# Kernel optimization log

Measured on AMD Instinct MI355X. Metric: run time of the kernel, lower is better.

## Reference

```python
import jax, jax.numpy as jnp
from jax import lax
import numpy as np

DIMNUMS = ('NCHW', 'OIHW', 'NCHW')
SCORE_THR = 0.6
IOU_THR = 0.5
STRIDE, CELL = 2.0, 12.0
IMG_OFFSET = 1.0e5  # > max coord, separates images for batched NMS


def _conv(x, w, b):
    y = lax.conv_general_dilated(x, w, (1, 1), 'VALID', dimension_numbers=DIMNUMS)
    return y + b[None, :, None, None]


def _prelu(x, a):
    return jnp.where(x >= 0, x, a[None, :, None, None] * x)


def _maxpool2_ceil(x):
    # MaxPool2d(2,2,ceil_mode=True): pad right/bottom so out = ceil(H/2)
    H, W = x.shape[2], x.shape[3]
    ph, pw = (-H) % 2, (-W) % 2
    return lax.reduce_window(x, -jnp.inf, lax.max, (1, 1, 2, 2), (1, 1, 2, 2),
                             [(0, 0), (0, 0), (0, ph), (0, pw)])


def _pnet(x, w1, b1, a1, w2, b2, a2, w3, b3, a3, w41, b41, w42, b42):
    h = _prelu(_conv(x, w1, b1), a1)
    h = _maxpool2_ceil(h)
    h = _prelu(_conv(h, w2, b2), a2)
    h = _prelu(_conv(h, w3, b3), a3)
    logits = _conv(h, w41, b41)            # [B,2,Hp,Wp]
    prob = jax.nn.softmax(logits, axis=1)[:, 1]  # [B,Hp,Wp]
    pred = _conv(h, w42, b42)              # [B,4,Hp,Wp]
    return pred, prob


def _greedy_nms(boxes, valid, thr):
    # boxes already sorted by descending score; valid marks admissible rows
    K = boxes.shape[0]
    x1, y1, x2, y2 = boxes[:, 0], boxes[:, 1], boxes[:, 2], boxes[:, 3]
    areas = (x2 - x1) * (y2 - y1)
    idxs = jnp.arange(K)

    def body(i, keep):
        bi = boxes[i]
        xx1 = jnp.maximum(bi[0], x1)
        yy1 = jnp.maximum(bi[1], y1)
        xx2 = jnp.minimum(bi[2], x2)
        yy2 = jnp.minimum(bi[3], y2)
        inter = jnp.maximum(xx2 - xx1, 0.0) * jnp.maximum(yy2 - yy1, 0.0)
        iou = inter / (areas[i] + areas - inter)
        sup = (iou > thr) & (idxs > i)
        return jnp.where(keep[i], keep & ~sup, keep)

    return lax.fori_loop(0, K, body, valid)


def _refine_bbox(boxes, pred):
    # plus_one=False variant (PNet stage)
    w = boxes[:, 2] - boxes[:, 0]
    h = boxes[:, 3] - boxes[:, 1]
    scale = jnp.stack([w, h, w, h], axis=1)
    return boxes + pred * scale


def _square_bbox(boxes):
    w = boxes[:, 2] - boxes[:, 0]
    h = boxes[:, 3] - boxes[:, 1]
    l = jnp.maximum(w, h)
    x1 = boxes[:, 0] + 0.5 * w - 0.5 * l
    y1 = boxes[:, 1] + 0.5 * h - 0.5 * l
    return jnp.stack([x1, y1, x1 + l, y1 + l], axis=1)


def setup_inputs() -> dict:
    key = jax.random.key(0)
    ks = jax.random.split(key, 16)
    B, H, W = 4, 1080, 1920
    f32 = jnp.float32
    d = {
        'x': jax.random.normal(ks[0], (B, 3, H, W), dtype=f32),
        'w1': jax.random.normal(ks[1], (10, 3, 3, 3), dtype=f32) * 0.1,
        'b1': jax.random.normal(ks[2], (10,), dtype=f32) * 0.1,
        'a1': jnp.full((10,), 0.25, dtype=f32),
        'w2': jax.random.normal(ks[3], (16, 10, 3, 3), dtype=f32) * 0.1,
        'b2': jax.random.normal(ks[4], (16,), dtype=f32) * 0.1,
        'a2': jnp.full((16,), 0.25, dtype=f32),
        'w3': jax.random.normal(ks[5], (32, 16, 3, 3), dtype=f32) * 0.1,
        'b3': jax.random.normal(ks[6], (32,), dtype=f32) * 0.1,
        'a3': jnp.full((32,), 0.25, dtype=f32),
        'w41': jax.random.normal(ks[7], (2, 32, 1, 1), dtype=f32) * 0.1,
        'b41': jax.random.normal(ks[8], (2,), dtype=f32) * 0.1,
        'w42': jax.random.normal(ks[9], (4, 32, 1, 1), dtype=f32) * 0.1,
        'b42': jax.random.normal(ks[10], (4,), dtype=f32) * 0.1,
        'k': 1024,
    }
    return d


def reference(x, w1, b1, a1, w2, b2, a2, w3, b3, a3, w41, b41, w42, b42, k):
    B = x.shape[0]
    pred, prob = _pnet(x, w1, b1, a1, w2, b2, a2, w3, b3, a3, w41, b41, w42, b42)
    Hp, Wp = prob.shape[1], prob.shape[2]

    # decode grid boxes: bb = (x=j, y=i); q1 = floor((2*bb+1)/scale), scale=1
    ys, xs = jnp.meshgrid(jnp.arange(Hp, dtype=jnp.float32),
                          jnp.arange(Wp, dtype=jnp.float32), indexing='ij')
    x1 = jnp.floor(STRIDE * xs + 1.0)
    y1 = jnp.floor(STRIDE * ys + 1.0)
    x2 = jnp.floor(STRIDE * xs + CELL)
    y2 = jnp.floor(STRIDE * ys + CELL)
    grid_boxes = jnp.stack([x1, y1, x2, y2], axis=-1).reshape(-1, 4)  # [Hp*Wp,4]

    N = Hp * Wp
    scores = prob.reshape(B * N)
    preds = pred.transpose(0, 2, 3, 1).reshape(B * N, 4)
    boxes = jnp.broadcast_to(grid_boxes[None], (B, N, 4)).reshape(B * N, 4)
    imgidx = jnp.repeat(jnp.arange(B), N)

    valid = scores >= SCORE_THR
    masked = jnp.where(valid, scores, -jnp.inf)
    vals, idx = lax.top_k(masked, k)

    tb = boxes[idx]
    tp = preds[idx]
    timg = imgidx[idx]
    tvalid = valid[idx]

    # batched NMS via per-image coordinate offset
    off = timg.astype(jnp.float32)[:, None] * IMG_OFFSET
    keep = _greedy_nms(tb + off, tvalid, IOU_THR)

    refined = _square_bbox(_refine_bbox(tb, tp))
    out = jnp.concatenate([refined, vals[:, None]], axis=1)  # [K,5]
    return jnp.where(keep[:, None], out, 0.0)
```

## Files before the change

### kernel.cpp

```cpp
#include <hip/hip_runtime.h>
#include <stdint.h>

using u32 = unsigned int;
using u64 = unsigned long long;

constexpr int BATCH = 4;
constexpr int H0 = 1080, W0 = 1920;
constexpr int HP = 539,  WP = 959;
constexpr int H2 = 537,  W2 = 957;
constexpr int H3 = 535,  W3 = 955;
constexpr int N3 = H3 * W3;
constexpr int TOT3 = BATCH * N3;
constexpr int KSEL = 1024;
constexpr int SORTCAP = 4096;
constexpr float SCORE_THR_C = 0.6f;
constexpr float IOU_THR_C = 0.5f;
constexpr float IMG_OFF = 100000.0f;

constexpr int T1RY = 34, T1CX = 30;
constexpr int C2TY = 34, C2TX = 30;
constexpr int C3TY = 34, C3TX = 30;

constexpr size_t align256(size_t x) { return (x + 255) & ~(size_t)255; }
constexpr size_t oP1   = 0;
constexpr size_t sP1   = (size_t)BATCH * 10 * HP * WP * 4;
constexpr size_t oC2   = align256(oP1 + sP1);
constexpr size_t sC2   = (size_t)BATCH * 16 * H2 * W2 * 4;
constexpr size_t oCand = align256(oC2 + sC2);
constexpr size_t sCand = (size_t)TOT3 * 8;
constexpr size_t oSort = align256(oCand + sCand);
constexpr size_t oSel  = align256(oSort + (size_t)SORTCAP * 8);
constexpr size_t oBox  = align256(oSel + (size_t)KSEL * 8);
constexpr size_t oSup  = align256(oBox + (size_t)KSEL * 16);
constexpr size_t oKeep = align256(oSup + (size_t)KSEL * 16 * 8);
constexpr size_t oMisc = align256(oKeep + 16 * 8);
constexpr int    MISC_WORDS = 16 + 2048;
constexpr size_t WS_NEEDED = oMisc + (size_t)MISC_WORDS * 4;

__device__ __forceinline__ int keybin(u64 key) {
  u32 khi = (u32)(key >> 32);
  int d = (int)(khi - 0xC0800000u);
  if (d < 0) d = 0;
  int bin = d >> 12;
  return bin > 2047 ? 2047 : bin;
}

__global__ __launch_bounds__(256) void k_conv1(
    const float* __restrict__ x, const float* __restrict__ w1,
    const float* __restrict__ b1, const float* __restrict__ a1,
    float* __restrict__ P1, u32* __restrict__ misc) {
  __shared__ float sm[6834];
  int tid = threadIdx.x;
  int blk = blockIdx.x;
  if (blk == 0) {
    for (int i = tid; i < MISC_WORDS; i += 256) misc[i] = 0;
  }
  int btx = blk % T1CX; int r1 = blk / T1CX; int bty = r1 % T1RY; int b = r1 / T1RY;
  int r0 = 16 * bty; if (r0 > 523) r0 = 523;
  int c0 = 32 * btx; if (c0 > 927) c0 = 927;

  const float* xb = x + (size_t)b * 3 * H0 * W0;
  for (int i = tid; i < 6732; i += 256) {
    int ci = i / 2244; int rem = i - ci * 2244; int row = rem / 66; int col = rem - row * 66;
    sm[ci * 2278 + row * 67 + col] =
        xb[(size_t)ci * H0 * W0 + (size_t)(2 * r0 + row) * W0 + (2 * c0 + col)];
  }
  __syncthreads();

  int pr = tid >> 4, pc = tid & 15;
  float acc[10][8];
  #pragma unroll
  for (int c = 0; c < 10; ++c) {
    float bb = b1[c];
    #pragma unroll
    for (int o = 0; o < 8; ++o) acc[c][o] = bb;
  }
  #pragma unroll 1
  for (int ci = 0; ci < 3; ++ci) {
    const float* sp = sm + ci * 2278 + (2 * pr) * 67 + 4 * pc;
    float in[4][6];
    #pragma unroll
    for (int iy = 0; iy < 4; ++iy)
      #pragma unroll
      for (int ix = 0; ix < 6; ++ix)
        in[iy][ix] = sp[iy * 67 + ix];
    #pragma unroll
    for (int c = 0; c < 10; ++c) {
      const float* wc = w1 + (c * 3 + ci) * 9;
      float w0v = wc[0], w1v = wc[1], w2v = wc[2], w3v = wc[3], w4v = wc[4],
            w5v = wc[5], w6v = wc[6], w7v = wc[7], w8v = wc[8];
      #pragma unroll
      for (int sr = 0; sr < 2; ++sr)
        #pragma unroll
        for (int sc = 0; sc < 4; ++sc) {
          float a = acc[c][sr * 4 + sc];
          a = fmaf(in[sr][sc],     w0v, a); a = fmaf(in[sr][sc+1],   w1v, a); a = fmaf(in[sr][sc+2],   w2v, a);
          a = fmaf(in[sr+1][sc],   w3v, a); a = fmaf(in[sr+1][sc+1], w4v, a); a = fmaf(in[sr+1][sc+2], w5v, a);
          a = fmaf(in[sr+2][sc],   w6v, a); a = fmaf(in[sr+2][sc+1], w7v, a); a = fmaf(in[sr+2][sc+2], w8v, a);
          acc[c][sr * 4 + sc] = a;
        }
    }
  }
  int gy = r0 + pr, gx = c0 + 2 * pc;
  size_t base = ((size_t)(b * 10) * HP + gy) * WP + gx;
  #pragma unroll
  for (int c = 0; c < 10; ++c) {
    float al = a1[c];
    float v[8];
    #pragma unroll
    for (int o = 0; o < 8; ++o) { float u = acc[c][o]; v[o] = u >= 0.0f ? u : al * u; }
    float m0 = fmaxf(fmaxf(v[0], v[1]), fmaxf(v[4], v[5]));
    float m1 = fmaxf(fmaxf(v[2], v[3]), fmaxf(v[6], v[7]));
    P1[base + (size_t)c * HP * WP]     = m0;
    P1[base + (size_t)c * HP * WP + 1] = m1;
  }
}

__global__ __launch_bounds__(256) void k_conv2(
    const float* __restrict__ P1, const float* __restrict__ w2,
    const float* __restrict__ b2, const float* __restrict__ a2,
    float* __restrict__ C2) {
  __shared__ float sm[6300];
  int tid = threadIdx.x;
  int blk = blockIdx.x;
  int tx = blk % C2TX; int r1 = blk / C2TX; int ty = r1 % C2TY; int b = r1 / C2TY;
  int r0 = 16 * ty; if (r0 > 521) r0 = 521;
  int c0 = 32 * tx; if (c0 > 925) c0 = 925;

  const float* Pb = P1 + (size_t)b * 10 * HP * WP;
  for (int i = tid; i < 6120; i += 256) {
    int ci = i / 612; int rem = i - ci * 612; int row = rem / 34; int col = rem - row * 34;
    sm[ci * 630 + row * 35 + col] =
        Pb[(size_t)ci * HP * WP + (size_t)(r0 + row) * WP + (c0 + col)];
  }
  __syncthreads();

  int lane = tid & 63;
  int wv = __builtin_amdgcn_readfirstlane(tid >> 6);
  int c_lo = wv * 4;
  int rr = lane >> 3;
  int gg = lane & 7;

  float acc[4][8];
  #pragma unroll
  for (int c = 0; c < 4; ++c) {
    float bb = b2[c_lo + c];
    #pragma unroll
    for (int o = 0; o < 8; ++o) acc[c][o] = bb;
  }
  #pragma unroll 1
  for (int ci = 0; ci < 10; ++ci) {
    const float* sp = sm + ci * 630 + (2 * rr) * 35 + 4 * gg;
    float in[4][6];
    #pragma unroll
    for (int dy = 0; dy < 4; ++dy)
      #pragma unroll
      for (int dx = 0; dx < 6; ++dx)
        in[dy][dx] = sp[dy * 35 + dx];
    #pragma unroll
    for (int c = 0; c < 4; ++c) {
      const float* wc = w2 + ((c_lo + c) * 10 + ci) * 9;
      float w0v = wc[0], w1v = wc[1], w2v = wc[2], w3v = wc[3], w4v = wc[4],
            w5v = wc[5], w6v = wc[6], w7v = wc[7], w8v = wc[8];
      #pragma unroll
      for (int d = 0; d < 2; ++d)
        #pragma unroll
        for (int k = 0; k < 4; ++k) {
          float a = acc[c][d * 4 + k];
          a = fmaf(in[d][k],   w0v, a); a = fmaf(in[d][k+1],   w1v, a); a = fmaf(in[d][k+2],   w2v, a);
          a = fmaf(in[d+1][k], w3v, a); a = fmaf(in[d+1][k+1], w4v, a); a = fmaf(in[d+1][k+2], w5v, a);
          a = fmaf(in[d+2][k], w6v, a); a = fmaf(in[d+2][k+1], w7v, a); a = fmaf(in[d+2][k+2], w8v, a);
          acc[c][d * 4 + k] = a;
        }
    }
  }
  #pragma unroll
  for (int c = 0; c < 4; ++c) {
    float al = a2[c_lo + c];
    #pragma unroll
    for (int d = 0; d < 2; ++d) {
      int gy = r0 + 2 * rr + d;
      size_t base = ((size_t)(b * 16 + c_lo + c) * H2 + gy) * W2 + (c0 + 4 * gg);
      #pragma unroll
      for (int k = 0; k < 4; ++k) {
        float v = acc[c][d * 4 + k];
        C2[base + k] = v >= 0.0f ? v : al * v;
      }
    }
  }
}

__device__ __forceinline__ void conv3_h(
    const float* __restrict__ C2, const float* __restrict__ w3,
    const float* __restrict__ b3, const float* __restrict__ a3,
    int b, int y, int x, float* h) {
  #pragma unroll
  for (int c = 0; c < 32; ++c) h[c] = b3[c];
  #pragma unroll 1
  for (int ci = 0; ci < 16; ++ci) {
    const float* p = C2 + ((size_t)(b * 16 + ci) * H2 + y) * W2 + x;
    float i0 = p[0],      i1 = p[1],      i2 = p[2];
    float i3 = p[W2],     i4 = p[W2+1],   i5 = p[W2+2];
    float i6 = p[2*W2],   i7 = p[2*W2+1], i8 = p[2*W2+2];
    const float* wp = w3 + ci * 9;
    #pragma unroll
    for (int c = 0; c < 32; ++c) {
      const float* wc = wp + c * 144;
      h[c] = fmaf(i0, wc[0], h[c]); h[c] = fmaf(i1, wc[1], h[c]);
      h[c] = fmaf(i2, wc[2], h[c]); h[c] = fmaf(i3, wc[3], h[c]);
      h[c] = fmaf(i4, wc[4], h[c]); h[c] = fmaf(i5, wc[5], h[c]);
      h[c] = fmaf(i6, wc[6], h[c]); h[c] = fmaf(i7, wc[7], h[c]);
      h[c] = fmaf(i8, wc[8], h[c]);
    }
  }
  #pragma unroll
  for (int c = 0; c < 32; ++c) h[c] = h[c] >= 0.0f ? h[c] : a3[c] * h[c];
}

__global__ __launch_bounds__(256) void k_conv3(
    const float* __restrict__ C2, const float* __restrict__ w3,
    const float* __restrict__ b3, const float* __restrict__ a3,
    const float* __restrict__ w41, const float* __restrict__ b41,
    u64* __restrict__ cands, u32* __restrict__ misc) {
  __shared__ __align__(16) float sm[10080];
  int tid = threadIdx.x;
  int blk = blockIdx.x;
  int tx = blk % C3TX; int r1 = blk / C3TX; int ty = r1 % C3TY; int b = r1 / C3TY;
  int ymin = 16 * ty, xmin = 32 * tx;
  int r0 = ymin > 519 ? 519 : ymin;
  int c0 = xmin > 923 ? 923 : xmin;

  const float* Cb = C2 + (size_t)b * 16 * H2 * W2;
  for (int i = tid; i < 9792; i += 256) {
    int ci = i / 612; int rem = i - ci * 612; int row = rem / 34; int col = rem - row * 34;
    sm[ci * 630 + row * 35 + col] =
        Cb[(size_t)ci * H2 * W2 + (size_t)(r0 + row) * W2 + (c0 + col)];
  }
  __syncthreads();

  int lane = tid & 63;
  int wv = __builtin_amdgcn_readfirstlane(tid >> 6);
  int c_lo = wv * 8;
  int rr = lane >> 3;
  int gg = lane & 7;

  float acc[8][8];
  #pragma unroll
  for (int c = 0; c < 8; ++c) {
    float bb = b3[c_lo + c];
    #pragma unroll
    for (int o = 0; o < 8; ++o) acc[c][o] = bb;
  }
  #pragma unroll 1
  for (int ci = 0; ci < 16; ++ci) {
    const float* sp = sm + ci * 630 + (2 * rr) * 35 + 4 * gg;
    float in[4][6];
    #pragma unroll
    for (int dy = 0; dy < 4; ++dy)
      #pragma unroll
      for (int dx = 0; dx < 6; ++dx)
        in[dy][dx] = sp[dy * 35 + dx];
    #pragma unroll
    for (int c = 0; c < 8; ++c) {
      const float* wc = w3 + ((c_lo + c) * 16 + ci) * 9;
      float w0v = wc[0], w1v = wc[1], w2v = wc[2], w3v = wc[3], w4v = wc[4],
            w5v = wc[5], w6v = wc[6], w7v = wc[7], w8v = wc[8];
      #pragma unroll
      for (int d = 0; d < 2; ++d)
        #pragma unroll
        for (int k = 0; k < 4; ++k) {
          float a = acc[c][d * 4 + k];
          a = fmaf(in[d][k],   w0v, a); a = fmaf(in[d][k+1],   w1v, a); a = fmaf(in[d][k+2],   w2v, a);
          a = fmaf(in[d+1][k], w3v, a); a = fmaf(in[d+1][k+1], w4v, a); a = fmaf(in[d+1][k+2], w5v, a);
          a = fmaf(in[d+2][k], w6v, a); a = fmaf(in[d+2][k+1], w7v, a); a = fmaf(in[d+2][k+2], w8v, a);
          acc[c][d * 4 + k] = a;
        }
    }
  }
  #pragma unroll
  for (int c = 0; c < 8; ++c) {
    float al = a3[c_lo + c];
    #pragma unroll
    for (int o = 0; o < 8; ++o) {
      float v = acc[c][o];
      acc[c][o] = v >= 0.0f ? v : al * v;
    }
  }
  __syncthreads();

  #pragma unroll
  for (int halfp = 0; halfp < 2; ++halfp) {
    if ((rr >> 2) == halfp) {
      #pragma unroll
      for (int c = 0; c < 8; ++c)
        #pragma unroll
        for (int d = 0; d < 2; ++d) {
          int row = 2 * rr + d - 8 * halfp;
          int word = (c_lo + c) * 256 + row * 32 + 4 * gg;
          *(float4*)&sm[word] = make_float4(acc[c][d*4+0], acc[c][d*4+1], acc[c][d*4+2], acc[c][d*4+3]);
        }
    }
    __syncthreads();
    {
      int p = tid;
      float l0 = b41[0], l1 = b41[1];
      #pragma unroll
      for (int c = 0; c < 32; ++c) {
        float hv = sm[c * 256 + p];
        l0 = fmaf(hv, w41[c],      l0);
        l1 = fmaf(hv, w41[32 + c], l1);
      }
      float prob = 1.0f / (1.0f + expf(l0 - l1));
      int gy = r0 + 8 * halfp + (p >> 5);
      int gx = c0 + (p & 31);
      if (prob >= SCORE_THR_C && gy >= ymin && gx >= xmin) {
        u32 idx = (u32)(b * N3 + gy * W3 + gx);
        u64 key = ((u64)(~__float_as_uint(prob)) << 32) | idx;
        atomicAdd(&misc[16 + keybin(key)], 1u);
        u32 pos = atomicAdd(&misc[0], 1u);
        cands[pos] = key;
      }
    }
    __syncthreads();
  }
}

__global__ __launch_bounds__(256) void k_compact(const u64* __restrict__ cands,
                                                u32* __restrict__ misc,
                                                u64* __restrict__ sortbuf) {
  __shared__ u32 lh[2048];
  __shared__ u32 part[256];
  __shared__ u32 sb;
  int tid = threadIdx.x;
  const u32* hist = misc + 16;
  for (int t = tid; t < 2048; t += 256) lh[t] = hist[t];
  __syncthreads();
  u32 s = 0;
  #pragma unroll
  for (int k = 0; k < 8; ++k) s += lh[tid * 8 + k];
  part[tid] = s;
  __syncthreads();
  if (tid == 0) {
    u32 total = misc[0]; if (total > (u32)TOT3) total = TOT3;
    u32 keff = total < (u32)KSEL ? total : (u32)KSEL;
    u32 run = 0; int chunk = 255;
    for (int t = 0; t < 256; ++t) {
      if (run + part[t] >= keff) { chunk = t; break; }
      run += part[t];
    }
    int bstar = 2047;
    for (int b = chunk * 8; b < chunk * 8 + 8; ++b) {
      u32 hv = lh[b];
      if (run + hv >= keff) { bstar = b; break; }
      run += hv;
    }
    sb = (u32)bstar;
    if (blockIdx.x == 0) { misc[2] = (u32)bstar; misc[3] = keff; }
  }
  __syncthreads();
  int bstar = (int)sb;
  u32 n = misc[0]; if (n > (u32)TOT3) n = TOT3;
  u32 stride = gridDim.x * 256;
  for (u32 i = blockIdx.x * 256 + tid; i < n; i += stride) {
    u64 key = cands[i];
    if (keybin(key) <= bstar) {
      u32 pos = atomicAdd(&misc[1], 1u);
      if (pos < (u32)SORTCAP) sortbuf[pos] = key;
    }
  }
}

__global__ __launch_bounds__(1024) void k_sort(const u64* __restrict__ sortbuf,
                                               const u32* __restrict__ misc,
                                               u64* __restrict__ selected,
                                               float4* __restrict__ boxarr) {
  __shared__ u64 s[SORTCAP];
  int tid = threadIdx.x;
  u32 nsel = misc[1]; if (nsel > (u32)SORTCAP) nsel = SORTCAP;
  unsigned m = KSEL;
  while (m < nsel) m <<= 1;
  for (int t = tid; t < (int)m; t += 1024) s[t] = (t < (int)nsel) ? sortbuf[t] : ~0ULL;
  for (unsigned k = 2; k <= m; k <<= 1) {
    for (unsigned j = k >> 1; j > 0; j >>= 1) {
      __syncthreads();
      for (int t = tid; t < (int)m; t += 1024) {
        int ixj = t ^ (int)j;
        if (ixj > t) {
          u64 a = s[t], b = s[ixj];
          bool up = ((t & (int)k) == 0);
          if ((a > b) == up) { s[t] = b; s[ixj] = a; }
        }
      }
    }
  }
  __syncthreads();
  if (tid < KSEL) {
    u64 key = s[tid];
    selected[tid] = key;
    u32 idx = (u32)key;
    u32 b = idx / (u32)N3;
    u32 rem = idx - b * (u32)N3;
    u32 y = rem / (u32)W3;
    u32 x = rem - y * (u32)W3;
    float off = (float)b * IMG_OFF;
    float x1 = (float)(2 * (int)x + 1) + off;
    float y1 = (float)(2 * (int)y + 1) + off;
    boxarr[tid] = make_float4(x1, y1, x1 + 11.0f, y1 + 11.0f);
  }
}

__global__ __launch_bounds__(256) void k_sup(const float4* __restrict__ boxarr,
                                             u64* __restrict__ sup) {
  __shared__ float4 lbox[KSEL];
  int tid = threadIdx.x;
  for (int t = tid; t < KSEL; t += 256) lbox[t] = boxarr[t];
  __syncthreads();
  int i = blockIdx.x * 16 + (tid >> 4);
  int w = tid & 15;
  float4 bi = lbox[i];
  float ai = (bi.z - bi.x) * (bi.w - bi.y);
  u64 m = 0;
  #pragma unroll 4
  for (int jj = 0; jj < 64; ++jj) {
    int j = (w << 6) + jj;
    float4 bj = lbox[j];
    float xx1 = fmaxf(bi.x, bj.x), yy1 = fmaxf(bi.y, bj.y);
    float xx2 = fminf(bi.z, bj.z), yy2 = fminf(bi.w, bj.w);
    float inter = fmaxf(xx2 - xx1, 0.0f) * fmaxf(yy2 - yy1, 0.0f);
    float aj = (bj.z - bj.x) * (bj.w - bj.y);
    float iou = inter / (ai + aj - inter);
    if (iou > IOU_THR_C && j > i) m |= (1ULL << jj);
  }
  sup[(size_t)i * 16 + w] = m;
}

__global__ __launch_bounds__(256) void k_nms(const u64* __restrict__ sup,
                                             const u32* __restrict__ misc,
                                             u64* __restrict__ keep) {
  __shared__ u64 lsup[512 * 16];
  __shared__ u64 rem[16];
  __shared__ u64 keepres[16];
  int tid = threadIdx.x;
  int lane = tid & 63;
  int total = (int)misc[3];
  if (tid < 16) {
    rem[tid] = 0;
    int nb = total - tid * 64;
    keepres[tid] = nb >= 64 ? ~0ULL : (nb <= 0 ? 0ULL : ((1ULL << nb) - 1ULL));
  }
  for (int chunk = 0; chunk < 2; ++chunk) {
    for (int t = tid; t < 512 * 16; t += 256) lsup[t] = sup[(size_t)chunk * 512 * 16 + t];
    __syncthreads();
    for (int jb = 0; jb < 8; ++jb) {
      int j = chunk * 8 + jb;
      if (tid < 64) {
        u64 intra = lsup[(jb * 64 + lane) * 16 + j];
        u64 kw = keepres[j] & ~rem[j];
        #pragma unroll 8
        for (int bbit = 0; bbit < 64; ++bbit) {
          u64 row = __shfl(intra, bbit);
          if ((kw >> bbit) & 1ULL) kw &= ~row;
        }
        if (lane == 0) keepres[j] = kw;
      }
      __syncthreads();
      if (tid < 16) {
        u64 kw = keepres[j];
        u64 r = rem[tid];
        int base = jb * 64;
        while (kw) {
          int bbit = __ffsll(kw) - 1;
          kw &= kw - 1;
          r |= lsup[(base + bbit) * 16 + tid];
        }
        rem[tid] = r;
      }
      __syncthreads();
    }
  }
  if (tid < 16) keep[tid] = keepres[tid];
}

__global__ __launch_bounds__(256) void k_emit(
    const float* __restrict__ C2, const float* __restrict__ w3,
    const float* __restrict__ b3, const float* __restrict__ a3,
    const float* __restrict__ w42, const float* __restrict__ b42,
    const u64* __restrict__ selected, const u64* __restrict__ keep,
    float* __restrict__ out) {
  int r = blockIdx.x * 256 + threadIdx.x;
  if (r >= KSEL) return;
  bool kb = (keep[r >> 6] >> (r & 63)) & 1ULL;
  if (!kb) {
    out[r*5+0] = 0.0f; out[r*5+1] = 0.0f; out[r*5+2] = 0.0f;
    out[r*5+3] = 0.0f; out[r*5+4] = 0.0f;
    return;
  }
  u64 key = selected[r];
  float score = __uint_as_float(~(u32)(key >> 32));
  u32 idx = (u32)key;
  int b = (int)(idx / (u32)N3);
  int rem = (int)(idx - (u32)b * (u32)N3);
  int y = rem / W3;
  int x = rem - y * W3;
  float h[32];
  conv3_h(C2, w3, b3, a3, b, y, x, h);
  float p0 = b42[0], p1 = b42[1], p2 = b42[2], p3 = b42[3];
  #pragma unroll
  for (int c = 0; c < 32; ++c) {
    p0 = fmaf(h[c], w42[c],      p0);
    p1 = fmaf(h[c], w42[32 + c], p1);
    p2 = fmaf(h[c], w42[64 + c], p2);
    p3 = fmaf(h[c], w42[96 + c], p3);
  }
  float x1 = (float)(2 * x + 1), y1f = (float)(2 * y + 1);
  float x2 = (float)(2 * x + 12), y2f = (float)(2 * y + 12);
  float bw = x2 - x1, bh = y2f - y1f;
  float rx1 = fmaf(p0, bw, x1), ry1 = fmaf(p1, bh, y1f);
  float rx2 = fmaf(p2, bw, x2), ry2 = fmaf(p3, bh, y2f);
  float rw = rx2 - rx1, rh = ry2 - ry1;
  float l = fmaxf(rw, rh);
  float ox1 = rx1 + 0.5f * rw - 0.5f * l;
  float oy1 = ry1 + 0.5f * rh - 0.5f * l;
  out[r*5+0] = ox1; out[r*5+1] = oy1;
  out[r*5+2] = ox1 + l; out[r*5+3] = oy1 + l;
  out[r*5+4] = score;
}

extern "C" void kernel_launch(void* const* d_in, const int* in_sizes, int n_in,
                              void* d_out, int out_size, void* d_ws, size_t ws_size,
                              hipStream_t stream) {
  if (ws_size < WS_NEEDED) return;
  const float* x   = (const float*)d_in[0];
  const float* w1  = (const float*)d_in[1];
  const float* b1  = (const float*)d_in[2];
  const float* a1  = (const float*)d_in[3];
  const float* w2  = (const float*)d_in[4];
  const float* b2  = (const float*)d_in[5];
  const float* a2  = (const float*)d_in[6];
  const float* w3  = (const float*)d_in[7];
  const float* b3  = (const float*)d_in[8];
  const float* a3  = (const float*)d_in[9];
  const float* w41 = (const float*)d_in[10];
  const float* b41 = (const float*)d_in[11];
  const float* w42 = (const float*)d_in[12];
  const float* b42 = (const float*)d_in[13];

  char* ws = (char*)d_ws;
  float*  P1       = (float*)(ws + oP1);
  float*  C2       = (float*)(ws + oC2);
  u64*    cands    = (u64*)(ws + oCand);
  u64*    sortbuf  = (u64*)(ws + oSort);
  u64*    selected = (u64*)(ws + oSel);
  float4* boxarr   = (float4*)(ws + oBox);
  u64*    sup      = (u64*)(ws + oSup);
  u64*    keep     = (u64*)(ws + oKeep);
  u32*    misc     = (u32*)(ws + oMisc);
  float*  out      = (float*)d_out;

  k_conv1<<<T1RY * T1CX * BATCH, 256, 0, stream>>>(x, w1, b1, a1, P1, misc);
  k_conv2<<<C2TX * C2TY * BATCH, 256, 0, stream>>>(P1, w2, b2, a2, C2);
  k_conv3<<<C3TX * C3TY * BATCH, 256, 0, stream>>>(C2, w3, b3, a3, w41, b41, cands, misc);
  k_compact<<<512, 256, 0, stream>>>(cands, misc, sortbuf);
  k_sort<<<1, 1024, 0, stream>>>(sortbuf, misc, selected, boxarr);
  k_sup<<<64, 256, 0, stream>>>(boxarr, sup);
  k_nms<<<1, 256, 0, stream>>>(sup, misc, keep);
  k_emit<<<(KSEL + 255) / 256, 256, 0, stream>>>(C2, w3, b3, a3, w42, b42, selected, keep, out);
}
```

Before: 618.5 us.

## Fuse compact, sort, suppression-mask and NMS kernels into one single-block tail kernel

```diff
diff --git a/kernel.cpp b/kernel.cpp
--- a/kernel.cpp
+++ b/kernel.cpp
@@ -28,11 +28,8 @@
 constexpr size_t sC2   = (size_t)BATCH * 16 * H2 * W2 * 4;
 constexpr size_t oCand = align256(oC2 + sC2);
 constexpr size_t sCand = (size_t)TOT3 * 8;
-constexpr size_t oSort = align256(oCand + sCand);
-constexpr size_t oSel  = align256(oSort + (size_t)SORTCAP * 8);
-constexpr size_t oBox  = align256(oSel + (size_t)KSEL * 8);
-constexpr size_t oSup  = align256(oBox + (size_t)KSEL * 16);
-constexpr size_t oKeep = align256(oSup + (size_t)KSEL * 16 * 8);
+constexpr size_t oSel  = align256(oCand + sCand);
+constexpr size_t oKeep = align256(oSel + (size_t)KSEL * 8);
 constexpr size_t oMisc = align256(oKeep + 16 * 8);
 constexpr int    MISC_WORDS = 16 + 2048;
 constexpr size_t WS_NEEDED = oMisc + (size_t)MISC_WORDS * 4;
@@ -325,20 +322,29 @@
   }
 }
 
-__global__ __launch_bounds__(256) void k_compact(const u64* __restrict__ cands,
-                                                u32* __restrict__ misc,
-                                                u64* __restrict__ sortbuf) {
-  __shared__ u32 lh[2048];
-  __shared__ u32 part[256];
-  __shared__ u32 sb;
+__global__ __launch_bounds__(1024) void k_tail(
+    const u64* __restrict__ cands, u32* __restrict__ misc,
+    u64* __restrict__ selected, u64* __restrict__ keep) {
+  __shared__ __align__(16) char smraw[99328];
+  u64*    sbuf = (u64*)smraw;
+  u64*    lsup = (u64*)(smraw + 8192);
+  float4* lbox = (float4*)(smraw + 73728);
+  u32*    lh   = (u32*)(smraw + 90112);
+  u32*    part = (u32*)(smraw + 98304);
+  __shared__ u32 s_bstar, s_keff, s_cnt;
+  __shared__ u64 remw[16], keepres[16];
   int tid = threadIdx.x;
-  const u32* hist = misc + 16;
-  for (int t = tid; t < 2048; t += 256) lh[t] = hist[t];
-  __syncthreads();
-  u32 s = 0;
-  #pragma unroll
-  for (int k = 0; k < 8; ++k) s += lh[tid * 8 + k];
-  part[tid] = s;
+  int lane = tid & 63;
+
+  for (int t = tid; t < 2048; t += 1024) lh[t] = misc[16 + t];
+  if (tid == 0) s_cnt = 0;
+  __syncthreads();
+  if (tid < 256) {
+    u32 s = 0;
+    #pragma unroll
+    for (int k = 0; k < 8; ++k) s += lh[tid * 8 + k];
+    part[tid] = s;
+  }
   __syncthreads();
   if (tid == 0) {
     u32 total = misc[0]; if (total > (u32)TOT3) total = TOT3;
@@ -354,48 +360,45 @@
       if (run + hv >= keff) { bstar = b; break; }
       run += hv;
     }
-    sb = (u32)bstar;
-    if (blockIdx.x == 0) { misc[2] = (u32)bstar; misc[3] = keff; }
-  }
-  __syncthreads();
-  int bstar = (int)sb;
-  u32 n = misc[0]; if (n > (u32)TOT3) n = TOT3;
-  u32 stride = gridDim.x * 256;
-  for (u32 i = blockIdx.x * 256 + tid; i < n; i += stride) {
-    u64 key = cands[i];
-    if (keybin(key) <= bstar) {
-      u32 pos = atomicAdd(&misc[1], 1u);
-      if (pos < (u32)SORTCAP) sortbuf[pos] = key;
-    }
-  }
-}
-
-__global__ __launch_bounds__(1024) void k_sort(const u64* __restrict__ sortbuf,
-                                               const u32* __restrict__ misc,
-                                               u64* __restrict__ selected,
-                                               float4* __restrict__ boxarr) {
-  __shared__ u64 s[SORTCAP];
-  int tid = threadIdx.x;
-  u32 nsel = misc[1]; if (nsel > (u32)SORTCAP) nsel = SORTCAP;
+    s_bstar = (u32)bstar;
+    s_keff = keff;
+  }
+  __syncthreads();
+
+  {
+    int bstar = (int)s_bstar;
+    u32 n = misc[0]; if (n > (u32)TOT3) n = TOT3;
+    for (u32 i = tid; i < n; i += 1024) {
+      u64 key = cands[i];
+      if (keybin(key) <= bstar) {
+        u32 pos = atomicAdd(&s_cnt, 1u);
+        if (pos < (u32)SORTCAP) sbuf[pos] = key;
+      }
+    }
+  }
+  __syncthreads();
+
+  u32 nsel = s_cnt; if (nsel > (u32)SORTCAP) nsel = SORTCAP;
   unsigned m = KSEL;
   while (m < nsel) m <<= 1;
-  for (int t = tid; t < (int)m; t += 1024) s[t] = (t < (int)nsel) ? sortbuf[t] : ~0ULL;
+  for (int t = tid; t < (int)m; t += 1024) if (t >= (int)nsel) sbuf[t] = ~0ULL;
+  __syncthreads();
   for (unsigned k = 2; k <= m; k <<= 1) {
     for (unsigned j = k >> 1; j > 0; j >>= 1) {
-      __syncthreads();
       for (int t = tid; t < (int)m; t += 1024) {
         int ixj = t ^ (int)j;
         if (ixj > t) {
-          u64 a = s[t], b = s[ixj];
+          u64 a = sbuf[t], b = sbuf[ixj];
           bool up = ((t & (int)k) == 0);
-          if ((a > b) == up) { s[t] = b; s[ixj] = a; }
-        }
-      }
-    }
-  }
-  __syncthreads();
-  if (tid < KSEL) {
-    u64 key = s[tid];
+          if ((a > b) == up) { sbuf[t] = b; sbuf[ixj] = a; }
+        }
+      }
+      __syncthreads();
+    }
+  }
+
+  {
+    u64 key = sbuf[tid];
     selected[tid] = key;
     u32 idx = (u32)key;
     u32 b = idx / (u32)N3;
@@ -405,57 +408,45 @@
     float off = (float)b * IMG_OFF;
     float x1 = (float)(2 * (int)x + 1) + off;
     float y1 = (float)(2 * (int)y + 1) + off;
-    boxarr[tid] = make_float4(x1, y1, x1 + 11.0f, y1 + 11.0f);
-  }
-}
-
-__global__ __launch_bounds__(256) void k_sup(const float4* __restrict__ boxarr,
-                                             u64* __restrict__ sup) {
-  __shared__ float4 lbox[KSEL];
-  int tid = threadIdx.x;
-  for (int t = tid; t < KSEL; t += 256) lbox[t] = boxarr[t];
-  __syncthreads();
-  int i = blockIdx.x * 16 + (tid >> 4);
-  int w = tid & 15;
-  float4 bi = lbox[i];
-  float ai = (bi.z - bi.x) * (bi.w - bi.y);
-  u64 m = 0;
-  #pragma unroll 4
-  for (int jj = 0; jj < 64; ++jj) {
-    int j = (w << 6) + jj;
-    float4 bj = lbox[j];
-    float xx1 = fmaxf(bi.x, bj.x), yy1 = fmaxf(bi.y, bj.y);
-    float xx2 = fminf(bi.z, bj.z), yy2 = fminf(bi.w, bj.w);
-    float inter = fmaxf(xx2 - xx1, 0.0f) * fmaxf(yy2 - yy1, 0.0f);
-    float aj = (bj.z - bj.x) * (bj.w - bj.y);
-    float iou = inter / (ai + aj - inter);
-    if (iou > IOU_THR_C && j > i) m |= (1ULL << jj);
-  }
-  sup[(size_t)i * 16 + w] = m;
-}
-
-__global__ __launch_bounds__(256) void k_nms(const u64* __restrict__ sup,
-                                             const u32* __restrict__ misc,
-                                             u64* __restrict__ keep) {
-  __shared__ u64 lsup[512 * 16];
-  __shared__ u64 rem[16];
-  __shared__ u64 keepres[16];
-  int tid = threadIdx.x;
-  int lane = tid & 63;
-  int total = (int)misc[3];
-  if (tid < 16) {
-    rem[tid] = 0;
-    int nb = total - tid * 64;
-    keepres[tid] = nb >= 64 ? ~0ULL : (nb <= 0 ? 0ULL : ((1ULL << nb) - 1ULL));
-  }
+    lbox[tid] = make_float4(x1, y1, x1 + 11.0f, y1 + 11.0f);
+  }
+  {
+    int total = (int)s_keff;
+    if (tid < 16) {
+      remw[tid] = 0;
+      int nb = total - tid * 64;
+      keepres[tid] = nb >= 64 ? ~0ULL : (nb <= 0 ? 0ULL : ((1ULL << nb) - 1ULL));
+    }
+  }
+  __syncthreads();
+
   for (int chunk = 0; chunk < 2; ++chunk) {
-    for (int t = tid; t < 512 * 16; t += 256) lsup[t] = sup[(size_t)chunk * 512 * 16 + t];
+    for (int task = tid; task < 8192; task += 1024) {
+      int i = task >> 4;
+      int w = task & 15;
+      int ir = chunk * 512 + i;
+      float4 bi = lbox[ir];
+      float ai = (bi.z - bi.x) * (bi.w - bi.y);
+      u64 msk = 0;
+      #pragma unroll 4
+      for (int jj = 0; jj < 64; ++jj) {
+        int j = (w << 6) + jj;
+        float4 bj = lbox[j];
+        float xx1 = fmaxf(bi.x, bj.x), yy1 = fmaxf(bi.y, bj.y);
+        float xx2 = fminf(bi.z, bj.z), yy2 = fminf(bi.w, bj.w);
+        float inter = fmaxf(xx2 - xx1, 0.0f) * fmaxf(yy2 - yy1, 0.0f);
+        float aj = (bj.z - bj.x) * (bj.w - bj.y);
+        float iou = inter / (ai + aj - inter);
+        if (iou > IOU_THR_C && j > ir) msk |= (1ULL << jj);
+      }
+      lsup[(size_t)i * 16 + w] = msk;
+    }
     __syncthreads();
     for (int jb = 0; jb < 8; ++jb) {
       int j = chunk * 8 + jb;
       if (tid < 64) {
         u64 intra = lsup[(jb * 64 + lane) * 16 + j];
-        u64 kw = keepres[j] & ~rem[j];
+        u64 kw = keepres[j] & ~remw[j];
         #pragma unroll 8
         for (int bbit = 0; bbit < 64; ++bbit) {
           u64 row = __shfl(intra, bbit);
@@ -466,14 +457,14 @@
       __syncthreads();
       if (tid < 16) {
         u64 kw = keepres[j];
-        u64 r = rem[tid];
+        u64 r = remw[tid];
         int base = jb * 64;
         while (kw) {
           int bbit = __ffsll(kw) - 1;
           kw &= kw - 1;
           r |= lsup[(base + bbit) * 16 + tid];
         }
-        rem[tid] = r;
+        remw[tid] = r;
       }
       __syncthreads();
     }
@@ -549,10 +540,7 @@
   float*  P1       = (float*)(ws + oP1);
   float*  C2       = (float*)(ws + oC2);
   u64*    cands    = (u64*)(ws + oCand);
-  u64*    sortbuf  = (u64*)(ws + oSort);
   u64*    selected = (u64*)(ws + oSel);
-  float4* boxarr   = (float4*)(ws + oBox);
-  u64*    sup      = (u64*)(ws + oSup);
   u64*    keep     = (u64*)(ws + oKeep);
   u32*    misc     = (u32*)(ws + oMisc);
   float*  out      = (float*)d_out;
@@ -560,9 +548,6 @@
   k_conv1<<<T1RY * T1CX * BATCH, 256, 0, stream>>>(x, w1, b1, a1, P1, misc);
   k_conv2<<<C2TX * C2TY * BATCH, 256, 0, stream>>>(P1, w2, b2, a2, C2);
   k_conv3<<<C3TX * C3TY * BATCH, 256, 0, stream>>>(C2, w3, b3, a3, w41, b41, cands, misc);
-  k_compact<<<512, 256, 0, stream>>>(cands, misc, sortbuf);
-  k_sort<<<1, 1024, 0, stream>>>(sortbuf, misc, selected, boxarr);
-  k_sup<<<64, 256, 0, stream>>>(boxarr, sup);
-  k_nms<<<1, 256, 0, stream>>>(sup, misc, keep);
+  k_tail<<<1, 1024, 0, stream>>>(cands, misc, selected, keep);
   k_emit<<<(KSEL + 255) / 256, 256, 0, stream>>>(C2, w3, b3, a3, w42, b42, selected, keep, out);
 }
```

Measured after the change: 1.024 ms. +65.5%, slower.

## Fuse conv1+PReLU+maxpool into conv2 kernel, eliminating P1 intermediate buffer

Applied to the files above, without the earlier changes.

```diff
diff --git a/kernel.cpp b/kernel.cpp
--- a/kernel.cpp
+++ b/kernel.cpp
@@ -17,14 +17,11 @@
 constexpr float IOU_THR_C = 0.5f;
 constexpr float IMG_OFF = 100000.0f;
 
-constexpr int T1RY = 34, T1CX = 30;
 constexpr int C2TY = 34, C2TX = 30;
 constexpr int C3TY = 34, C3TX = 30;
 
 constexpr size_t align256(size_t x) { return (x + 255) & ~(size_t)255; }
-constexpr size_t oP1   = 0;
-constexpr size_t sP1   = (size_t)BATCH * 10 * HP * WP * 4;
-constexpr size_t oC2   = align256(oP1 + sP1);
+constexpr size_t oC2   = 0;
 constexpr size_t sC2   = (size_t)BATCH * 16 * H2 * W2 * 4;
 constexpr size_t oCand = align256(oC2 + sC2);
 constexpr size_t sCand = (size_t)TOT3 * 8;
@@ -45,93 +42,90 @@
   return bin > 2047 ? 2047 : bin;
 }
 
-__global__ __launch_bounds__(256) void k_conv1(
+__global__ __launch_bounds__(256) void k_conv12(
     const float* __restrict__ x, const float* __restrict__ w1,
     const float* __restrict__ b1, const float* __restrict__ a1,
-    float* __restrict__ P1, u32* __restrict__ misc) {
-  __shared__ float sm[6834];
+    const float* __restrict__ w2, const float* __restrict__ b2,
+    const float* __restrict__ a2,
+    float* __restrict__ C2, u32* __restrict__ misc) {
+  __shared__ float sm[8094];
   int tid = threadIdx.x;
   int blk = blockIdx.x;
   if (blk == 0) {
     for (int i = tid; i < MISC_WORDS; i += 256) misc[i] = 0;
   }
-  int btx = blk % T1CX; int r1 = blk / T1CX; int bty = r1 % T1RY; int b = r1 / T1RY;
-  int r0 = 16 * bty; if (r0 > 523) r0 = 523;
-  int c0 = 32 * btx; if (c0 > 927) c0 = 927;
-
-  const float* xb = x + (size_t)b * 3 * H0 * W0;
-  for (int i = tid; i < 6732; i += 256) {
-    int ci = i / 2244; int rem = i - ci * 2244; int row = rem / 66; int col = rem - row * 66;
-    sm[ci * 2278 + row * 67 + col] =
-        xb[(size_t)ci * H0 * W0 + (size_t)(2 * r0 + row) * W0 + (2 * c0 + col)];
-  }
-  __syncthreads();
-
-  int pr = tid >> 4, pc = tid & 15;
-  float acc[10][8];
-  #pragma unroll
-  for (int c = 0; c < 10; ++c) {
-    float bb = b1[c];
-    #pragma unroll
-    for (int o = 0; o < 8; ++o) acc[c][o] = bb;
-  }
-  #pragma unroll 1
-  for (int ci = 0; ci < 3; ++ci) {
-    const float* sp = sm + ci * 2278 + (2 * pr) * 67 + 4 * pc;
-    float in[4][6];
-    #pragma unroll
-    for (int iy = 0; iy < 4; ++iy)
-      #pragma unroll
-      for (int ix = 0; ix < 6; ++ix)
-        in[iy][ix] = sp[iy * 67 + ix];
-    #pragma unroll
-    for (int c = 0; c < 10; ++c) {
-      const float* wc = w1 + (c * 3 + ci) * 9;
-      float w0v = wc[0], w1v = wc[1], w2v = wc[2], w3v = wc[3], w4v = wc[4],
-            w5v = wc[5], w6v = wc[6], w7v = wc[7], w8v = wc[8];
-      #pragma unroll
-      for (int sr = 0; sr < 2; ++sr)
-        #pragma unroll
-        for (int sc = 0; sc < 4; ++sc) {
-          float a = acc[c][sr * 4 + sc];
-          a = fmaf(in[sr][sc],     w0v, a); a = fmaf(in[sr][sc+1],   w1v, a); a = fmaf(in[sr][sc+2],   w2v, a);
-          a = fmaf(in[sr+1][sc],   w3v, a); a = fmaf(in[sr+1][sc+1], w4v, a); a = fmaf(in[sr+1][sc+2], w5v, a);
-          a = fmaf(in[sr+2][sc],   w6v, a); a = fmaf(in[sr+2][sc+1], w7v, a); a = fmaf(in[sr+2][sc+2], w8v, a);
-          acc[c][sr * 4 + sc] = a;
-        }
-    }
-  }
-  int gy = r0 + pr, gx = c0 + 2 * pc;
-  size_t base = ((size_t)(b * 10) * HP + gy) * WP + gx;
-  #pragma unroll
-  for (int c = 0; c < 10; ++c) {
-    float al = a1[c];
-    float v[8];
-    #pragma unroll
-    for (int o = 0; o < 8; ++o) { float u = acc[c][o]; v[o] = u >= 0.0f ? u : al * u; }
-    float m0 = fmaxf(fmaxf(v[0], v[1]), fmaxf(v[4], v[5]));
-    float m1 = fmaxf(fmaxf(v[2], v[3]), fmaxf(v[6], v[7]));
-    P1[base + (size_t)c * HP * WP]     = m0;
-    P1[base + (size_t)c * HP * WP + 1] = m1;
-  }
-}
-
-__global__ __launch_bounds__(256) void k_conv2(
-    const float* __restrict__ P1, const float* __restrict__ w2,
-    const float* __restrict__ b2, const float* __restrict__ a2,
-    float* __restrict__ C2) {
-  __shared__ float sm[6300];
-  int tid = threadIdx.x;
-  int blk = blockIdx.x;
   int tx = blk % C2TX; int r1 = blk / C2TX; int ty = r1 % C2TY; int b = r1 / C2TY;
   int r0 = 16 * ty; if (r0 > 521) r0 = 521;
   int c0 = 32 * tx; if (c0 > 925) c0 = 925;
 
-  const float* Pb = P1 + (size_t)b * 10 * HP * WP;
-  for (int i = tid; i < 6120; i += 256) {
-    int ci = i / 612; int rem = i - ci * 612; int row = rem / 34; int col = rem - row * 34;
-    sm[ci * 630 + row * 35 + col] =
-        Pb[(size_t)ci * HP * WP + (size_t)(r0 + row) * WP + (c0 + col)];
+  const float* xb = x + (size_t)b * 3 * H0 * W0;
+  for (int i = tid; i < 7980; i += 256) {
+    int ci = i / 2660; int rem = i - ci * 2660; int row = rem / 70; int col = rem - row * 70;
+    sm[ci * 2698 + row * 71 + col] =
+        xb[(size_t)ci * H0 * W0 + (size_t)(2 * r0 + row) * W0 + (2 * c0 + col)];
+  }
+  __syncthreads();
+
+  float pool[3][10];
+  #pragma unroll
+  for (int it = 0; it < 3; ++it) {
+    int p = tid + it * 256;
+    if (p < 612) {
+      int py = p / 34, pxc = p - py * 34;
+      float accv[10][4];
+      #pragma unroll
+      for (int c = 0; c < 10; ++c) {
+        float bb = b1[c];
+        accv[c][0] = bb; accv[c][1] = bb; accv[c][2] = bb; accv[c][3] = bb;
+      }
+      #pragma unroll 1
+      for (int ci = 0; ci < 3; ++ci) {
+        const float* sp = sm + ci * 2698 + (2 * py) * 71 + 2 * pxc;
+        float in[4][4];
+        #pragma unroll
+        for (int dy = 0; dy < 4; ++dy)
+          #pragma unroll
+          for (int dx = 0; dx < 4; ++dx)
+            in[dy][dx] = sp[dy * 71 + dx];
+        #pragma unroll
+        for (int c = 0; c < 10; ++c) {
+          const float* wc = w1 + (c * 3 + ci) * 9;
+          float w0v = wc[0], w1v = wc[1], w2v = wc[2], w3v = wc[3], w4v = wc[4],
+                w5v = wc[5], w6v = wc[6], w7v = wc[7], w8v = wc[8];
+          #pragma unroll
+          for (int sy = 0; sy < 2; ++sy)
+            #pragma unroll
+            for (int sx = 0; sx < 2; ++sx) {
+              float a = accv[c][sy * 2 + sx];
+              a = fmaf(in[sy][sx],     w0v, a); a = fmaf(in[sy][sx+1],   w1v, a); a = fmaf(in[sy][sx+2],   w2v, a);
+              a = fmaf(in[sy+1][sx],   w3v, a); a = fmaf(in[sy+1][sx+1], w4v, a); a = fmaf(in[sy+1][sx+2], w5v, a);
+              a = fmaf(in[sy+2][sx],   w6v, a); a = fmaf(in[sy+2][sx+1], w7v, a); a = fmaf(in[sy+2][sx+2], w8v, a);
+              accv[c][sy * 2 + sx] = a;
+            }
+        }
+      }
+      #pragma unroll
+      for (int c = 0; c < 10; ++c) {
+        float al = a1[c];
+        float v0 = accv[c][0] >= 0.0f ? accv[c][0] : al * accv[c][0];
+        float v1 = accv[c][1] >= 0.0f ? accv[c][1] : al * accv[c][1];
+        float v2 = accv[c][2] >= 0.0f ? accv[c][2] : al * accv[c][2];
+        float v3 = accv[c][3] >= 0.0f ? accv[c][3] : al * accv[c][3];
+        pool[it][c] = fmaxf(fmaxf(v0, v1), fmaxf(v2, v3));
+      }
+    }
+  }
+  __syncthreads();
+
+  #pragma unroll
+  for (int it = 0; it < 3; ++it) {
+    int p = tid + it * 256;
+    if (p < 612) {
+      int py = p / 34, pxc = p - py * 34;
+      #pragma unroll
+      for (int c = 0; c < 10; ++c)
+        sm[c * 630 + py * 35 + pxc] = pool[it][c];
+    }
   }
   __syncthreads();
 
@@ -546,7 +540,6 @@
   const float* b42 = (const float*)d_in[13];
 
   char* ws = (char*)d_ws;
-  float*  P1       = (float*)(ws + oP1);
   float*  C2       = (float*)(ws + oC2);
   u64*    cands    = (u64*)(ws + oCand);
   u64*    sortbuf  = (u64*)(ws + oSort);
@@ -557,8 +550,7 @@
   u32*    misc     = (u32*)(ws + oMisc);
   float*  out      = (float*)d_out;
 
-  k_conv1<<<T1RY * T1CX * BATCH, 256, 0, stream>>>(x, w1, b1, a1, P1, misc);
-  k_conv2<<<C2TX * C2TY * BATCH, 256, 0, stream>>>(P1, w2, b2, a2, C2);
+  k_conv12<<<C2TX * C2TY * BATCH, 256, 0, stream>>>(x, w1, b1, a1, w2, b2, a2, C2, misc);
   k_conv3<<<C3TX * C3TY * BATCH, 256, 0, stream>>>(C2, w3, b3, a3, w41, b41, cands, misc);
   k_compact<<<512, 256, 0, stream>>>(cands, misc, sortbuf);
   k_sort<<<1, 1024, 0, stream>>>(sortbuf, misc, selected, boxarr);
```

Measured after the change: 570.9 us. 7.7% less time.
